# Kernel optimization log

Measured on AMD Instinct MI355X. Metric: run time of the kernel, lower is better.

## Reference

```python
import jax, jax.numpy as jnp
import numpy as np

B, D_IN, D_OUT, S = 8192, 1024, 4096, 64
C = D_OUT // S          # chunk size per seed = 64
H = 2 * C               # blueprint hidden = 128


def setup_inputs() -> dict:
    key = jax.random.key(0)
    ks = jax.random.split(key, 9)
    sc = lambda *shape: 1.0 / np.sqrt(shape[-1] if len(shape) > 1 else 1.0)
    x = jax.random.normal(ks[0], (B, D_IN), jnp.float32)
    Wb = jax.random.normal(ks[1], (D_OUT, D_IN), jnp.float32) * (1.0 / np.sqrt(D_IN))
    bb = jax.random.normal(ks[2], (D_OUT,), jnp.float32) * 0.01
    W1 = jax.random.normal(ks[3], (S, C, H), jnp.float32) * (1.0 / np.sqrt(C))
    b1 = jax.random.normal(ks[4], (S, H), jnp.float32) * 0.01
    W2 = jax.random.normal(ks[5], (S, H, C), jnp.float32) * (1.0 / np.sqrt(H))
    b2 = jax.random.normal(ks[6], (S, C), jnp.float32) * 0.01
    alpha = jax.random.uniform(ks[7], (S,), jnp.float32)
    active = jax.random.randint(ks[8], (S,), 0, 2) > 0  # bool mask of active seeds
    return {"x": x, "Wb": Wb, "bb": bb, "W1": W1, "b1": b1,
            "W2": W2, "b2": b2, "alpha": alpha, "active": active}


def reference(x, Wb, bb, W1, b1, W2, b2, alpha, active):
    # base layer: Linear(D_IN -> D_OUT)
    base = x @ Wb.T + bb                       # [B, D_OUT]
    y = base.reshape(B, S, C)                  # chunked view: [B, S, C]
    # per-seed blueprint MLP: Linear(C, 2C) -> ReLU -> Linear(2C, C), grouped over seeds
    h = jax.nn.relu(jnp.einsum('bsc,sch->bsh', y, W1) + b1)   # [B, S, H]
    bp = jnp.einsum('bsh,shc->bsc', h, W2) + b2               # [B, S, C]
    # alpha-blend only for active seeds; inactive seeds pass chunk through
    a = (alpha * active.astype(alpha.dtype))[None, :, None]    # [1, S, 1]
    out = (1.0 - a) * y + a * bp               # [B, S, C]
    return out.reshape(B, D_OUT)
```

## Files before the change

kernel.cpp:

```cpp
#include <hip/hip_runtime.h>
#include <stdint.h>

typedef unsigned short u16;
typedef __bf16 bf16x8 __attribute__((ext_vector_type(8)));
typedef unsigned short u16x8 __attribute__((ext_vector_type(8)));
typedef u16x8 u16x8_ma __attribute__((may_alias));
typedef unsigned short u16x4 __attribute__((ext_vector_type(4)));
typedef float f32x4 __attribute__((ext_vector_type(4)));

#define DIN   1024
#define DOUT  4096
#define BM    256
#define BN    256
#define BK    32
#define NTILE 32
#define BUFSZ 16384

__device__ __forceinline__ u16 f2bf(float f) {
  unsigned u = __float_as_uint(f);
  u += 0x7fffu + ((u >> 16) & 1u);
  return (u16)(u >> 16);
}
__device__ __forceinline__ bf16x8 ldfrag(const u16* p) {
  union { u16x8 u; bf16x8 b; } cv;
  cv.u = *(const u16x8_ma*)p;
  return cv.b;
}
__device__ __forceinline__ f32x4 mfma16(bf16x8 a, bf16x8 b, f32x4 c) {
  return __builtin_amdgcn_mfma_f32_16x16x32_bf16(a, b, c, 0, 0, 0);
}
__device__ __forceinline__ void gload_lds16(const u16* g, u16* l) {
  __builtin_amdgcn_global_load_lds(
      (const __attribute__((address_space(1))) void*)g,
      (__attribute__((address_space(3))) void*)l, 16, 0, 0);
}
__device__ __forceinline__ void wave_lds_fence() {
  __asm__ __volatile__("s_waitcnt lgkmcnt(0)" ::: "memory");
}

__global__ void prep_all(const float* __restrict__ X, const float* __restrict__ Wb,
                         const float* __restrict__ W1, const float* __restrict__ W2,
                         u16* __restrict__ Xb, u16* __restrict__ Wbb,
                         u16* __restrict__ W1T, u16* __restrict__ W2T) {
  __shared__ u16 tile[8192];
  const int b = blockIdx.x;
  const int t = threadIdx.x;

  if (b < 3072) {
    const float* src; u16* dst; int n4, i, stride;
    if (b < 2048) { src = X;  dst = Xb;  n4 = (8192 * 1024) / 4; i = b * 256 + t;          stride = 2048 * 256; }
    else          { src = Wb; dst = Wbb; n4 = (4096 * 1024) / 4; i = (b - 2048) * 256 + t; stride = 1024 * 256; }
    for (; i < n4; i += stride) {
      f32x4 v = ((const f32x4*)src)[i];
      u16x4 o;
      o.x = f2bf(v.x); o.y = f2bf(v.y); o.z = f2bf(v.z); o.w = f2bf(v.w);
      ((u16x4*)dst)[i] = o;
    }
    return;
  }

  const int s = b - 3072;
  const float* w1 = W1 + s * 8192;
  u16* w1t = W1T + s * 8192;
  for (int i = t; i < 8192; i += 256) tile[i] = f2bf(w1[i]);
  __syncthreads();
  for (int i = t; i < 8192; i += 256) {
    int h = i >> 6, c = i & 63;
    w1t[i] = tile[c * 128 + h];
  }
  __syncthreads();

  const float* w2 = W2 + s * 8192;
  u16* w2t = W2T + s * 8192;
  for (int i = t; i < 8192; i += 256) tile[i] = f2bf(w2[i]);
  __syncthreads();
  for (int i = t; i < 8192; i += 256) {
    int c = i >> 7, h = i & 127;
    w2t[i] = tile[h * 64 + c];
  }
}

__global__ __launch_bounds__(512, 2) void kasmina_fused(
    const u16* __restrict__ X,   const u16* __restrict__ Wb,
    const float* __restrict__ bb,  const float* __restrict__ b1,
    const float* __restrict__ b2,  const float* __restrict__ alpha,
    const int* __restrict__ active,
    const u16* __restrict__ W1T, const u16* __restrict__ W2T,
    float* __restrict__ out)
{
  __shared__ u16 lds[65536];

  const int t = threadIdx.x;
  const int w = t >> 6, l = t & 63;
  const int wm = w >> 2, wn = w & 3;
  const int lane15 = l & 15, quad = l >> 4;
  const int bn0 = blockIdx.x * BN;
  const int bm0 = blockIdx.y * BM;

  f32x4 acc[8][4];
#pragma unroll
  for (int mt = 0; mt < 8; ++mt)
#pragma unroll
    for (int nt = 0; nt < 4; ++nt)
      acc[mt][nt] = (f32x4){0.f, 0.f, 0.f, 0.f};

  const int rl = l >> 2;
  const int cs = ((l & 3) ^ ((l >> 3) & 3)) << 3;
  const u16* Ag = X  + (size_t)(bm0 + w * 16 + rl) * DIN + cs;
  const u16* Bg = Wb + (size_t)(bn0 + w * 16 + rl) * DIN + cs;

  const int swz = (quad ^ ((lane15 >> 1) & 3)) << 3;
  const int aoff = (wm * 128 + lane15) * 32 + swz;
  const int boff = 8192 + (wn * 64 + lane15) * 32 + swz;

#pragma unroll
  for (int tt = 0; tt < 3; ++tt) {
    const int k0 = tt * BK;
    u16* dst = &lds[tt * BUFSZ];
    gload_lds16(Ag + k0,                    dst + w * 512);
    gload_lds16(Ag + (size_t)128 * DIN + k0, dst + 4096 + w * 512);
    gload_lds16(Bg + k0,                    dst + 8192 + w * 512);
    gload_lds16(Bg + (size_t)128 * DIN + k0, dst + 12288 + w * 512);
  }
  __asm__ __volatile__("s_waitcnt vmcnt(8)" ::: "memory");
  __builtin_amdgcn_s_barrier();

#pragma unroll 1
  for (int j = 0; j < NTILE; ++j) {
    const u16* bufp = &lds[(j & 3) * BUFSZ];
    const int stg = (j + 3) & 3;
    const int k0n = (j + 3) * BK;

    bf16x8 bfr[4], afr[4], afr2[4];
#pragma unroll
    for (int nt = 0; nt < 4; ++nt) bfr[nt] = ldfrag(bufp + boff + nt * 512);
#pragma unroll
    for (int mt = 0; mt < 4; ++mt) afr[mt] = ldfrag(bufp + aoff + mt * 512);
    if (j < NTILE - 3) {
      u16* dst = &lds[stg * BUFSZ];
      gload_lds16(Ag + k0n,                     dst + w * 512);
      gload_lds16(Ag + (size_t)128 * DIN + k0n, dst + 4096 + w * 512);
    }
    __builtin_amdgcn_s_barrier();
    __builtin_amdgcn_s_setprio(1);
#pragma unroll
    for (int mt = 0; mt < 4; ++mt)
#pragma unroll
      for (int nt = 0; nt < 4; ++nt)
        acc[mt][nt] = mfma16(afr[mt], bfr[nt], acc[mt][nt]);
    __builtin_amdgcn_s_setprio(0);
    __builtin_amdgcn_s_barrier();

#pragma unroll
    for (int mt = 0; mt < 4; ++mt) afr2[mt] = ldfrag(bufp + aoff + (mt + 4) * 512);
    if (j < NTILE - 3) {
      u16* dst = &lds[stg * BUFSZ];
      gload_lds16(Bg + k0n,                     dst + 8192 + w * 512);
      gload_lds16(Bg + (size_t)128 * DIN + k0n, dst + 12288 + w * 512);
    }
    if (j < NTILE - 3)       { __asm__ __volatile__("s_waitcnt vmcnt(8)" ::: "memory"); }
    else if (j == NTILE - 3) { __asm__ __volatile__("s_waitcnt vmcnt(4)" ::: "memory"); }
    else if (j == NTILE - 2) { __asm__ __volatile__("s_waitcnt vmcnt(0)" ::: "memory"); }
    __builtin_amdgcn_s_barrier();
    __builtin_amdgcn_s_setprio(1);
#pragma unroll
    for (int mt = 0; mt < 4; ++mt)
#pragma unroll
      for (int nt = 0; nt < 4; ++nt)
        acc[mt + 4][nt] = mfma16(afr2[mt], bfr[nt], acc[mt + 4][nt]);
    __builtin_amdgcn_s_setprio(0);
    __builtin_amdgcn_s_barrier();
  }

  const int sidx = blockIdx.x * 4 + wn;
  const int act = active[sidx];
  float bbv[4];
#pragma unroll
  for (int nt = 0; nt < 4; ++nt) bbv[nt] = bb[sidx * 64 + nt * 16 + lane15];

  const size_t orow0 = (size_t)(bm0 + wm * 128);

  if (!act) {
#pragma unroll
    for (int mt = 0; mt < 8; ++mt)
#pragma unroll
      for (int nt = 0; nt < 4; ++nt) {
        f32x4 yv = acc[mt][nt];
        const int col = sidx * 64 + nt * 16 + lane15;
#pragma unroll
        for (int r = 0; r < 4; ++r) {
          const size_t row = orow0 + mt * 16 + quad * 4 + r;
          out[row * DOUT + col] = yv[r] + bbv[nt];
        }
      }
    return;
  }

  const float aval = alpha[sidx];

  u16* Yw = &lds[w * 4608];
  u16* Hw = Yw + 2304;

#pragma unroll
  for (int mh = 0; mh < 4; ++mh) {
#pragma unroll
    for (int mt = 0; mt < 2; ++mt)
#pragma unroll
      for (int nt = 0; nt < 4; ++nt) {
        f32x4 v = acc[mh * 2 + mt][nt];
        const int col = nt * 16 + lane15;
#pragma unroll
        for (int r = 0; r < 4; ++r)
          Yw[(mt * 16 + quad * 4 + r) * 72 + col] = f2bf(v[r] + bbv[nt]);
      }
    wave_lds_fence();

    f32x4 bp[2][4];
#pragma unroll
    for (int nt = 0; nt < 4; ++nt) {
      const float b2v = b2[sidx * 64 + nt * 16 + lane15];
      const f32x4 tv = (f32x4){b2v, b2v, b2v, b2v};
      bp[0][nt] = tv; bp[1][nt] = tv;
    }

#pragma unroll 1
    for (int hh = 0; hh < 2; ++hh) {
      f32x4 hc[2][4];
#pragma unroll
      for (int nt = 0; nt < 4; ++nt) {
        const float b1v = b1[sidx * 128 + hh * 64 + nt * 16 + lane15];
        const f32x4 tv = (f32x4){b1v, b1v, b1v, b1v};
        hc[0][nt] = tv; hc[1][nt] = tv;
      }
      const u16* w1b = W1T + sidx * 8192 + (hh * 64 + lane15) * 64 + quad * 8;
#pragma unroll
      for (int ks = 0; ks < 2; ++ks) {
        bf16x8 af0 = ldfrag(Yw + lane15 * 72 + ks * 32 + quad * 8);
        bf16x8 af1 = ldfrag(Yw + (16 + lane15) * 72 + ks * 32 + quad * 8);
#pragma unroll
        for (int nt = 0; nt < 4; ++nt) {
          bf16x8 bfr = ldfrag(w1b + nt * 1024 + ks * 32);
          hc[0][nt] = mfma16(af0, bfr, hc[0][nt]);
          hc[1][nt] = mfma16(af1, bfr, hc[1][nt]);
        }
      }
#pragma unroll
      for (int mt = 0; mt < 2; ++mt)
#pragma unroll
        for (int nt = 0; nt < 4; ++nt) {
          f32x4 v = hc[mt][nt];
          const int col = nt * 16 + lane15;
#pragma unroll
          for (int r = 0; r < 4; ++r) {
            float hv = v[r] > 0.f ? v[r] : 0.f;
            Hw[(mt * 16 + quad * 4 + r) * 72 + col] = f2bf(hv);
          }
        }
      wave_lds_fence();
      const u16* w2b = W2T + sidx * 8192 + lane15 * 128 + hh * 64 + quad * 8;
#pragma unroll
      for (int ks = 0; ks < 2; ++ks) {
        bf16x8 af0 = ldfrag(Hw + lane15 * 72 + ks * 32 + quad * 8);
        bf16x8 af1 = ldfrag(Hw + (16 + lane15) * 72 + ks * 32 + quad * 8);
#pragma unroll
        for (int nt = 0; nt < 4; ++nt) {
          bf16x8 bfr = ldfrag(w2b + nt * 2048 + ks * 32);
          bp[0][nt] = mfma16(af0, bfr, bp[0][nt]);
          bp[1][nt] = mfma16(af1, bfr, bp[1][nt]);
        }
      }
      wave_lds_fence();
    }
#pragma unroll
    for (int mt = 0; mt < 2; ++mt)
#pragma unroll
      for (int nt = 0; nt < 4; ++nt) {
        f32x4 yv = acc[mh * 2 + mt][nt];
        f32x4 pv = bp[mt][nt];
        const int col = sidx * 64 + nt * 16 + lane15;
#pragma unroll
        for (int r = 0; r < 4; ++r) {
          const float y = yv[r] + bbv[nt];
          const float o = (1.0f - aval) * y + aval * pv[r];
          const size_t row = orow0 + mh * 32 + mt * 16 + quad * 4 + r;
          out[row * DOUT + col] = o;
        }
      }
    wave_lds_fence();
  }
}

extern "C" void kernel_launch(void* const* d_in, const int* in_sizes, int n_in,
                              void* d_out, int out_size, void* d_ws, size_t ws_size,
                              hipStream_t stream) {
  const float* X     = (const float*)d_in[0];
  const float* Wb    = (const float*)d_in[1];
  const float* bbp   = (const float*)d_in[2];
  const float* W1    = (const float*)d_in[3];
  const float* b1p   = (const float*)d_in[4];
  const float* W2    = (const float*)d_in[5];
  const float* b2p   = (const float*)d_in[6];
  const float* alpha = (const float*)d_in[7];
  const int*  active = (const int*)d_in[8];
  float* out = (float*)d_out;

  u16* W1T = (u16*)d_ws;
  u16* W2T = W1T + 524288;
  u16* Xb  = W1T + 1048576;
  u16* Wbb = W1T + 9437184;

  prep_all<<<3136, 256, 0, stream>>>(X, Wb, W1, W2, Xb, Wbb, W1T, W2T);
  kasmina_fused<<<dim3(16, 32), 512, 0, stream>>>(
      Xb, Wbb, bbp, b1p, b2p, alpha, active, W1T, W2T, out);
}
```

Baseline: 297.4 us.

## Double-buffer register fragments in GEMM main loop and use nontemporal output stores

Restructures the base GEMM K-loop into a two-iteration unrolled ping-pong: fragments for the next K tile are read from LDS into a second register set while the MFMAs for the current tile run, and each K step is cut to one barrier pair instead of four barriers. Output writes now use nontemporal stores to avoid polluting cache with the large fp32 result. The cost is extra VGPR pressure from holding two full fragment sets (24 bf16x8 vectors), which could cause spills or lower occupancy.

```diff
diff --git a/kernel.cpp b/kernel.cpp
--- a/kernel.cpp
+++ b/kernel.cpp
@@ -113,64 +113,65 @@
   const int aoff = (wm * 128 + lane15) * 32 + swz;
   const int boff = 8192 + (wn * 64 + lane15) * 32 + swz;
 
-#pragma unroll
-  for (int tt = 0; tt < 3; ++tt) {
-    const int k0 = tt * BK;
-    u16* dst = &lds[tt * BUFSZ];
-    gload_lds16(Ag + k0,                    dst + w * 512);
-    gload_lds16(Ag + (size_t)128 * DIN + k0, dst + 4096 + w * 512);
-    gload_lds16(Bg + k0,                    dst + 8192 + w * 512);
-    gload_lds16(Bg + (size_t)128 * DIN + k0, dst + 12288 + w * 512);
-  }
-  __asm__ __volatile__("s_waitcnt vmcnt(8)" ::: "memory");
+#define VM4 __asm__ __volatile__("s_waitcnt vmcnt(4)" ::: "memory")
+#define VM0 __asm__ __volatile__("s_waitcnt vmcnt(0)" ::: "memory")
+#define VM8 __asm__ __volatile__("s_waitcnt vmcnt(8)" ::: "memory")
+
+#define STAGE(JP3) do {                                                  \
+    const int kk_ = (JP3) * BK;                                          \
+    u16* dst_ = &lds[((JP3) & 3) * BUFSZ];                               \
+    gload_lds16(Ag + kk_,          dst_ +         w * 512);              \
+    gload_lds16(Ag + 131072 + kk_, dst_ +  4096 + w * 512);              \
+    gload_lds16(Bg + kk_,          dst_ +  8192 + w * 512);              \
+    gload_lds16(Bg + 131072 + kk_, dst_ + 12288 + w * 512);              \
+  } while (0)
+
+#define READS(AF, BF, BI) do {                                           \
+    const u16* bufp_ = &lds[(BI) * BUFSZ];                               \
+    _Pragma("unroll")                                                    \
+    for (int nt_ = 0; nt_ < 4; ++nt_) BF[nt_] = ldfrag(bufp_ + boff + nt_ * 512); \
+    _Pragma("unroll")                                                    \
+    for (int mt_ = 0; mt_ < 8; ++mt_) AF[mt_] = ldfrag(bufp_ + aoff + mt_ * 512); \
+  } while (0)
+
+#define MFMAS(AF, BF) do {                                               \
+    __builtin_amdgcn_s_setprio(1);                                       \
+    _Pragma("unroll")                                                    \
+    for (int mt_ = 0; mt_ < 8; ++mt_)                                    \
+      _Pragma("unroll")                                                  \
+      for (int nt_ = 0; nt_ < 4; ++nt_)                                  \
+        acc[mt_][nt_] = mfma16(AF[mt_], BF[nt_], acc[mt_][nt_]);         \
+    __builtin_amdgcn_s_setprio(0);                                       \
+  } while (0)
+
+  bf16x8 afA[8], bfA[4], afB[8], bfB[4];
+
+  STAGE(0); STAGE(1); STAGE(2);
+  VM8;
   __builtin_amdgcn_s_barrier();
+  READS(afA, bfA, 0);
 
 #pragma unroll 1
-  for (int j = 0; j < NTILE; ++j) {
-    const u16* bufp = &lds[(j & 3) * BUFSZ];
-    const int stg = (j + 3) & 3;
-    const int k0n = (j + 3) * BK;
-
-    bf16x8 bfr[4], afr[4], afr2[4];
-#pragma unroll
-    for (int nt = 0; nt < 4; ++nt) bfr[nt] = ldfrag(bufp + boff + nt * 512);
-#pragma unroll
-    for (int mt = 0; mt < 4; ++mt) afr[mt] = ldfrag(bufp + aoff + mt * 512);
-    if (j < NTILE - 3) {
-      u16* dst = &lds[stg * BUFSZ];
-      gload_lds16(Ag + k0n,                     dst + w * 512);
-      gload_lds16(Ag + (size_t)128 * DIN + k0n, dst + 4096 + w * 512);
-    }
+  for (int jb = 0; jb < 30; jb += 2) {
+    VM4;
     __builtin_amdgcn_s_barrier();
-    __builtin_amdgcn_s_setprio(1);
-#pragma unroll
-    for (int mt = 0; mt < 4; ++mt)
-#pragma unroll
-      for (int nt = 0; nt < 4; ++nt)
-        acc[mt][nt] = mfma16(afr[mt], bfr[nt], acc[mt][nt]);
-    __builtin_amdgcn_s_setprio(0);
+    READS(afB, bfB, (jb + 1) & 3);
+    STAGE(jb + 3);
+    MFMAS(afA, bfA);
+
+    VM4;
     __builtin_amdgcn_s_barrier();
-
-#pragma unroll
-    for (int mt = 0; mt < 4; ++mt) afr2[mt] = ldfrag(bufp + aoff + (mt + 4) * 512);
-    if (j < NTILE - 3) {
-      u16* dst = &lds[stg * BUFSZ];
-      gload_lds16(Bg + k0n,                     dst + 8192 + w * 512);
-      gload_lds16(Bg + (size_t)128 * DIN + k0n, dst + 12288 + w * 512);
-    }
-    if (j < NTILE - 3)       { __asm__ __volatile__("s_waitcnt vmcnt(8)" ::: "memory"); }
-    else if (j == NTILE - 3) { __asm__ __volatile__("s_waitcnt vmcnt(4)" ::: "memory"); }
-    else if (j == NTILE - 2) { __asm__ __volatile__("s_waitcnt vmcnt(0)" ::: "memory"); }
-    __builtin_amdgcn_s_barrier();
-    __builtin_amdgcn_s_setprio(1);
-#pragma unroll
-    for (int mt = 0; mt < 4; ++mt)
-#pragma unroll
-      for (int nt = 0; nt < 4; ++nt)
-        acc[mt + 4][nt] = mfma16(afr2[mt], bfr[nt], acc[mt + 4][nt]);
-    __builtin_amdgcn_s_setprio(0);
-    __builtin_amdgcn_s_barrier();
-  }
+    READS(afA, bfA, (jb + 2) & 3);
+    if (jb < 28) STAGE(jb + 4);
+    MFMAS(afB, bfB);
+  }
+  VM0;
+  __builtin_amdgcn_s_barrier();
+  READS(afB, bfB, 3);
+  MFMAS(afA, bfA);
+  MFMAS(afB, bfB);
+
+  __builtin_amdgcn_s_barrier();
 
   const int sidx = blockIdx.x * 4 + wn;
   const int act = active[sidx];
@@ -190,7 +191,7 @@
 #pragma unroll
         for (int r = 0; r < 4; ++r) {
           const size_t row = orow0 + mt * 16 + quad * 4 + r;
-          out[row * DOUT + col] = yv[r] + bbv[nt];
+          __builtin_nontemporal_store(yv[r] + bbv[nt], &out[row * DOUT + col]);
         }
       }
     return;
@@ -283,7 +284,7 @@
           const float y = yv[r] + bbv[nt];
           const float o = (1.0f - aval) * y + aval * pv[r];
           const size_t row = orow0 + mh * 32 + mt * 16 + quad * 4 + r;
-          out[row * DOUT + col] = o;
+          __builtin_nontemporal_store(o, &out[row * DOUT + col]);
         }
       }
     wave_lds_fence();
@@ -296,8 +297,8 @@
   const float* X     = (const float*)d_in[0];
   const float* Wb    = (const float*)d_in[1];
   const float* bbp   = (const float*)d_in[2];
+  const float* b1p   = (const float*)d_in[4];
   const float* W1    = (const float*)d_in[3];
-  const float* b1p   = (const float*)d_in[4];
   const float* W2    = (const float*)d_in[5];
   const float* b2p   = (const float*)d_in[6];
   const float* alpha = (const float*)d_in[7];
```

Result: no change. 296.3 us (-0.4%).
